# Kernel optimization log

Measured on AMD Instinct MI355X. Metric: run time of the kernel, lower is better.

The kernel has to match this reference:

```python
import jax, jax.numpy as jnp
import numpy as np

SEQ_LEN = 131072
D_MODEL = 512
M = 1000
BETA = 0.5


def setup_inputs() -> dict:
    key = jax.random.key(0)
    k_t, k_m, k_wm, k_wt, k_bt = jax.random.split(key, 5)
    t = jax.random.normal(k_t, (SEQ_LEN,), dtype=jnp.float32)  # ~half negative -> masked
    marker = jax.random.randint(k_m, (SEQ_LEN,), 0, M, dtype=jnp.int32)
    W_m = jax.random.normal(k_wm, (D_MODEL, M), dtype=jnp.float32)
    W_t = jax.random.normal(k_wt, (D_MODEL,), dtype=jnp.float32)
    b_t = jax.random.normal(k_bt, (D_MODEL,), dtype=jnp.float32)
    return {"t": t, "marker": marker, "W_m": W_m, "W_t": W_t, "b_t": b_t}


def reference(t, marker, W_m, W_t, b_t):
    # one-hot matmul W_m @ one_hot(marker) == column gather of W_m -> row gather of W_m.T
    emb_m = jnp.take(W_m.T, marker, axis=0)            # [S, d_model]
    emb_t = t[:, None] * W_t[None, :] + b_t[None, :]   # [S, d_model]
    out = BETA * emb_m + (1.0 - BETA) * emb_t
    return jnp.where(t[:, None] < 0, jnp.zeros((), dtype=out.dtype), out)
```

## Files before the change

kernel.cpp:

```cpp
#include <hip/hip_runtime.h>

#define SEQ_LEN 131072
#define D_MODEL 512
#define M_SIZE  1000
#define BETA    0.5f

typedef float f32x4 __attribute__((ext_vector_type(4)));

__global__ void transpose_wm_kernel(const float* __restrict__ W_m,
                                    float* __restrict__ W_mT) {
    __shared__ float tile[32][33];
    const int bx = blockIdx.x;
    const int by = blockIdx.y;
    const int tx = threadIdx.x;
    const int ty = threadIdx.y;

    const int m = bx * 32 + tx;
    const int d0 = by * 32;
    for (int i = ty; i < 32; i += 8) {
        const int d = d0 + i;
        tile[i][tx] = (m < M_SIZE) ? W_m[(long)d * M_SIZE + m] : 0.0f;
    }
    __syncthreads();
    const int m0 = bx * 32;
    for (int i = ty; i < 32; i += 8) {
        const int mm = m0 + i;
        if (mm < M_SIZE) W_mT[(long)mm * D_MODEL + d0 + tx] = tile[tx][i];
    }
}

__global__ void embed_kernel(const float* __restrict__ t,
                             const int* __restrict__ marker,
                             const float* __restrict__ W_mT,
                             const float* __restrict__ W_t,
                             const float* __restrict__ b_t,
                             float* __restrict__ out) {
    const int c = threadIdx.x & 127;
    const int rowInBlock = threadIdx.x >> 7;
    const int sStride = (int)gridDim.x * 2;

    const f32x4 w = reinterpret_cast<const f32x4*>(W_t)[c];
    const f32x4 b = reinterpret_cast<const f32x4*>(b_t)[c];
    f32x4* __restrict__ out4 = reinterpret_cast<f32x4*>(out);

    int s = (int)blockIdx.x * 2 + rowInBlock;
    if (s >= SEQ_LEN) return;

    float tv = t[s];
    int   m  = marker[s];

    while (true) {
        const int sn = s + sStride;
        float tv_n = 0.0f;
        int   m_n  = 0;
        if (sn < SEQ_LEN) {
            tv_n = t[sn];
            m_n  = marker[sn];
        }

        f32x4 o;
        if (tv < 0.0f) {
            o = (f32x4)(0.0f);
        } else {
            const f32x4 em =
                reinterpret_cast<const f32x4*>(W_mT + (size_t)m * D_MODEL)[c];
            o.x = BETA * em.x + (1.0f - BETA) * fmaf(tv, w.x, b.x);
            o.y = BETA * em.y + (1.0f - BETA) * fmaf(tv, w.y, b.y);
            o.z = BETA * em.z + (1.0f - BETA) * fmaf(tv, w.z, b.z);
            o.w = BETA * em.w + (1.0f - BETA) * fmaf(tv, w.w, b.w);
        }
        __builtin_nontemporal_store(o, out4 + (size_t)s * (D_MODEL / 4) + c);

        if (sn >= SEQ_LEN) break;
        s = sn; tv = tv_n; m = m_n;
    }
}

extern "C" void kernel_launch(void* const* d_in, const int* in_sizes, int n_in,
                              void* d_out, int out_size, void* d_ws, size_t ws_size,
                              hipStream_t stream) {
    const float* t      = (const float*)d_in[0];
    const int*   marker = (const int*)d_in[1];
    const float* W_m    = (const float*)d_in[2];
    const float* W_t    = (const float*)d_in[3];
    const float* b_t    = (const float*)d_in[4];
    float* out = (float*)d_out;

    float* W_mT = (float*)d_ws;
    (void)ws_size;

    dim3 tgrid((M_SIZE + 31) / 32, D_MODEL / 32);
    dim3 tblock(32, 8);
    transpose_wm_kernel<<<tgrid, tblock, 0, stream>>>(W_m, W_mT);

    embed_kernel<<<2048, 256, 0, stream>>>(t, marker, W_mT, W_t, b_t, out);
}
```

Before: 57.73 us.

## Software-pipeline embedding gather two rows ahead with fixed trip count

Restructures the grid-stride loop into a fixed 32-iteration loop with compile-time stride 4096, prefetching t/marker two rows ahead and the W_mT gather one row ahead. The goal is to hide gather latency behind the current row's compute and store, and to let the compiler unroll without bounds checks. This hardcodes the 2048-block grid and SEQ_LEN geometry and adds register pressure.

```diff
diff --git a/kernel.cpp b/kernel.cpp
--- a/kernel.cpp
+++ b/kernel.cpp
@@ -29,50 +29,56 @@
     }
 }
 
-__global__ void embed_kernel(const float* __restrict__ t,
-                             const int* __restrict__ marker,
-                             const float* __restrict__ W_mT,
-                             const float* __restrict__ W_t,
-                             const float* __restrict__ b_t,
-                             float* __restrict__ out) {
+#define SSTRIDE 4096
+#define NITER   32
+
+__global__ __launch_bounds__(256) void
+embed_kernel(const float* __restrict__ t,
+             const int* __restrict__ marker,
+             const float* __restrict__ W_mT,
+             const float* __restrict__ W_t,
+             const float* __restrict__ b_t,
+             float* __restrict__ out) {
     const int c = threadIdx.x & 127;
     const int rowInBlock = threadIdx.x >> 7;
-    const int sStride = (int)gridDim.x * 2;
+    int s = (int)blockIdx.x * 2 + rowInBlock;
 
     const f32x4 w = reinterpret_cast<const f32x4*>(W_t)[c];
     const f32x4 b = reinterpret_cast<const f32x4*>(b_t)[c];
     f32x4* __restrict__ out4 = reinterpret_cast<f32x4*>(out);
+    const f32x4* __restrict__ wmT4 = reinterpret_cast<const f32x4*>(W_mT);
 
-    int s = (int)blockIdx.x * 2 + rowInBlock;
-    if (s >= SEQ_LEN) return;
+    float t0 = t[s];            int m0 = marker[s];
+    float t1 = t[s + SSTRIDE];  int m1 = marker[s + SSTRIDE];
 
-    float tv = t[s];
-    int   m  = marker[s];
+    f32x4 em0 = (f32x4)(0.0f);
+    if (t0 >= 0.0f) em0 = wmT4[(size_t)m0 * (D_MODEL / 4) + c];
 
-    while (true) {
-        const int sn = s + sStride;
-        float tv_n = 0.0f;
-        int   m_n  = 0;
-        if (sn < SEQ_LEN) {
-            tv_n = t[sn];
-            m_n  = marker[sn];
+    #pragma unroll 4
+    for (int i = 0; i < NITER; ++i) {
+        float t2 = 0.0f; int m2 = 0;
+        if (i < NITER - 2) {
+            const int s2 = s + 2 * SSTRIDE;
+            t2 = t[s2];
+            m2 = marker[s2];
         }
+        f32x4 em1 = (f32x4)(0.0f);
+        if (i < NITER - 1 && t1 >= 0.0f)
+            em1 = wmT4[(size_t)m1 * (D_MODEL / 4) + c];
 
-        f32x4 o;
-        if (tv < 0.0f) {
-            o = (f32x4)(0.0f);
-        } else {
-            const f32x4 em =
-                reinterpret_cast<const f32x4*>(W_mT + (size_t)m * D_MODEL)[c];
-            o.x = BETA * em.x + (1.0f - BETA) * fmaf(tv, w.x, b.x);
-            o.y = BETA * em.y + (1.0f - BETA) * fmaf(tv, w.y, b.y);
-            o.z = BETA * em.z + (1.0f - BETA) * fmaf(tv, w.z, b.z);
-            o.w = BETA * em.w + (1.0f - BETA) * fmaf(tv, w.w, b.w);
+        f32x4 o = (f32x4)(0.0f);
+        if (t0 >= 0.0f) {
+            o.x = BETA * em0.x + (1.0f - BETA) * fmaf(t0, w.x, b.x);
+            o.y = BETA * em0.y + (1.0f - BETA) * fmaf(t0, w.y, b.y);
+            o.z = BETA * em0.z + (1.0f - BETA) * fmaf(t0, w.z, b.z);
+            o.w = BETA * em0.w + (1.0f - BETA) * fmaf(t0, w.w, b.w);
         }
         __builtin_nontemporal_store(o, out4 + (size_t)s * (D_MODEL / 4) + c);
 
-        if (sn >= SEQ_LEN) break;
-        s = sn; tv = tv_n; m = m_n;
+        s += SSTRIDE;
+        t0 = t1; em0 = em1;
+        t1 = t2; m1 = m2;
+        (void)m0; m0 = m1;
     }
 }
 
```

After: 60.82 us. 5.3% more time.
